# Performance work log

Measured on AMD Instinct MI355X. Metric: run time of the kernel, lower is better.

Reference implementation:

```python
import jax, jax.numpy as jnp
import numpy as np
import math

# dims
H = 2048        # hidden_size
NH = 16         # mamba_num_heads
HPH = 128       # hidden_size_per_head
I = NH * HPH    # intermediate_size = 2048
N = 64          # mamba_d_state
K = 4           # mamba_d_conv
R = max(64, H // 16)  # time_step_rank = 128
L = 2048        # total tokens (single prefill sequence)
EPS = 1e-6


def rmsnorm(x, w, eps=EPS):
    return x * jax.lax.rsqrt(jnp.mean(x * x, axis=-1, keepdims=True) + eps) * w


def setup_inputs() -> dict:
    key = jax.random.key(0)
    ks = jax.random.split(key, 12)
    s = 0.02
    # dt_bias per get_initial_dt_bias
    dt_min, dt_max = 0.001, 0.1
    u = jax.random.uniform(ks[0], (NH,))
    dt = jnp.exp(u * (math.log(dt_max) - math.log(dt_min)) + math.log(dt_min))
    dt = jnp.clip(dt, 0.0001)
    dt_bias = dt + jnp.log(-jnp.expm1(-dt))
    return {
        "hidden_states": jax.random.normal(ks[1], (L, H), jnp.float32),
        "in_proj_w": jax.random.normal(ks[2], (H, 2 * I), jnp.float32) * s,
        "conv_w": jax.random.normal(ks[3], (I, K), jnp.float32) * s,
        "bcdt_w": jax.random.normal(ks[4], (I, 2 * N + R), jnp.float32) * s,
        "dt_norm_w": jnp.ones((R,), jnp.float32),
        "B_norm_w": jnp.ones((N,), jnp.float32),
        "C_norm_w": jnp.ones((N,), jnp.float32),
        "dt_proj_w": jax.random.normal(ks[5], (R, NH), jnp.float32) * s,
        "dt_bias": dt_bias.astype(jnp.float32),
        "A": -jnp.exp(jax.random.normal(ks[6], (I, N), jnp.float32) * 0.5),  # A = -exp(A_log)
        "D": jnp.ones((I,), jnp.float32),
        "out_proj_w": jax.random.normal(ks[7], (I, H), jnp.float32) * s,
    }


def reference(hidden_states, in_proj_w, conv_w, bcdt_w, dt_norm_w, B_norm_w,
              C_norm_w, dt_proj_w, dt_bias, A, D, out_proj_w):
    # in_proj -> [L, NH, 2*HPH]; split into gate and hidden (per-head halves)
    proj = (hidden_states @ in_proj_w).reshape(L, NH, 2 * HPH)
    gate = proj[:, :, :HPH].reshape(L, I)
    hs = proj[:, :, HPH:].reshape(L, I)

    # causal depthwise conv1d along time + SiLU
    xp = jnp.pad(hs, ((K - 1, 0), (0, 0)))  # left-pad time (zero initial conv state)
    conv = sum(conv_w[:, k] * xp[k:k + L] for k in range(K))  # [L, I]
    hs = jax.nn.silu(conv)

    # B, C, dt projections + RMSNorms
    ssm_p = hs @ bcdt_w  # [L, 2N+R]
    B = rmsnorm(ssm_p[:, :N], B_norm_w)          # [L, N]
    C = rmsnorm(ssm_p[:, N:2 * N], C_norm_w)     # [L, N]
    ts = rmsnorm(ssm_p[:, 2 * N:], dt_norm_w)    # [L, R]
    dt = ts @ dt_proj_w                           # [L, NH]

    # expand per-head dt / bias to full intermediate dim, softplus discretization
    dt_full = jnp.repeat(dt, HPH, axis=1)         # [L, I]
    bias_full = jnp.repeat(dt_bias, HPH)          # [I]
    delta = jax.nn.softplus(dt_full + bias_full)  # [L, I]

    # selective scan: state [I, N], zero initial state
    def step(state, xs):
        u_t, d_t, B_t, C_t = xs
        dA = jnp.exp(d_t[:, None] * A)                      # [I, N]
        state = state * dA + (d_t * u_t)[:, None] * B_t[None, :]
        y_t = state @ C_t                                    # [I]
        return state, y_t

    state0 = jnp.zeros((I, N), jnp.float32)
    _, ys = jax.lax.scan(step, state0, (hs, delta, B, C))    # ys: [L, I]

    y = ys + D * hs
    y = y * jax.nn.silu(gate)
    return y @ out_proj_w  # [L, H]
```

## Files before the change

kernel.cpp:

```cpp
#include <hip/hip_runtime.h>
#include <hip/hip_bf16.h>

#define L_   2048
#define H_   2048
#define I_   2048
#define NH_  16
#define HPH_ 128
#define NS_  64
#define R_   128
#define NCH_ 64
#define CT_  32
#define LOG2E 1.4426950408889634f

typedef __attribute__((ext_vector_type(8))) short s16x8;
typedef __attribute__((ext_vector_type(4))) float f32x4;

__device__ __forceinline__ short f2bf(float x) {
  unsigned u = __builtin_bit_cast(unsigned, x);
  u += 0x7fff + ((u >> 16) & 1);
  return (short)(u >> 16);
}
__device__ __forceinline__ float bf2f(unsigned short v) {
  return __builtin_bit_cast(float, (unsigned)v << 16);
}

__device__ __forceinline__ float ex2(float x) {
  return __builtin_amdgcn_exp2f(x);
}

__device__ __forceinline__ void gll16(const void* g, void* l) {
  __builtin_amdgcn_global_load_lds(
      (__attribute__((address_space(1))) void*)(void*)g,
      (__attribute__((address_space(3))) void*)l, 16, 0, 0);
}

__global__ __launch_bounds__(256) void pack_w(const float* __restrict__ W,
                                              short* __restrict__ Wp,
                                              int KN, int logN) {
  int idx = blockIdx.x * 256 + threadIdx.x;
  if (idx >= KN) return;
  int k = idx >> logN;
  int n = idx & ((1 << logN) - 1);
  Wp[((size_t)(k >> 3) << (logN + 3)) + ((size_t)n << 3) + (k & 7)] = f2bf(W[idx]);
}

__global__ __launch_bounds__(256) void cast_bf(const float* __restrict__ X,
                                               short* __restrict__ Xb, int nElem) {
  int idx = blockIdx.x * 256 + threadIdx.x;
  if (idx < nElem) Xb[idx] = f2bf(X[idx]);
}

template<int BM>
__global__ __launch_bounds__(256) void gemm_st(const short* __restrict__ A,
                                               const short* __restrict__ Bp,
                                               float* __restrict__ C,
                                               int M, int N, int K) {
  constexpr int MI = BM / 32;
  __shared__ short sA[BM * 64];
  __shared__ short sB[8 * 128 * 8];
  int tid = threadIdx.x;
  int lane = tid & 63, wid = tid >> 6;
  int wr = wid >> 1, wc = wid & 1;
  int l15 = lane & 15, l16 = lane >> 4;

  int nwg = gridDim.x * gridDim.y;
  int lin = blockIdx.x + gridDim.x * blockIdx.y;
  int cpx = nwg >> 3;
  int swz = (lin & 7) * cpx + (lin >> 3);
  int bm = (swz % gridDim.x) * BM, bn = (swz / gridDim.x) * 128;

  f32x4 acc[MI][4] = {};

  int arow = lane >> 3;
  int acolb = ((lane & 7) ^ arow) * 16;
  const char* Ag = (const char*)(A + (size_t)bm * K) + acolb;
  const char* Bg = (const char*)(Bp + (size_t)bn * 8);

  for (int k0 = 0; k0 < K; k0 += 64) {
    __syncthreads();
#pragma unroll
    for (int q = 0; q < BM / 32; ++q) {
      int rbase = (q * 4 + wid) * 8;
      gll16(Ag + ((size_t)(rbase + arow) * K + k0) * 2,
            (char*)sA + rbase * 128);
    }
#pragma unroll
    for (int q = 0; q < 4; ++q) {
      int c = q * 4 + wid;
      int kg = c >> 1, nh = (c & 1) * 64;
      gll16(Bg + ((size_t)(k0 / 8 + kg) * N * 8 + (size_t)(nh + lane) * 8) * 2,
            (char*)sB + kg * 2048 + nh * 16);
    }
    __syncthreads();

#pragma unroll
    for (int kk = 0; kk < 64; kk += 32) {
      s16x8 a[MI], b[4];
#pragma unroll
      for (int mi = 0; mi < MI; ++mi) {
        int row = wr * (BM / 2) + mi * 16 + l15;
        int kb = ((kk + l16 * 8) * 2) ^ ((row & 7) << 4);
        a[mi] = *(const s16x8*)((const char*)sA + row * 128 + kb);
      }
#pragma unroll
      for (int ni = 0; ni < 4; ++ni) {
        int n = wc * 64 + ni * 16 + l15;
        int kg = (kk >> 3) + l16;
        b[ni] = *(const s16x8*)((const char*)sB + (kg * 128 + n) * 16);
      }
#pragma unroll
      for (int mi = 0; mi < MI; ++mi)
#pragma unroll
        for (int ni = 0; ni < 4; ++ni)
          acc[mi][ni] = __builtin_amdgcn_mfma_f32_16x16x32_bf16(a[mi], b[ni], acc[mi][ni], 0, 0, 0);
    }
  }
#pragma unroll
  for (int mi = 0; mi < MI; ++mi) {
    int row0 = bm + wr * (BM / 2) + mi * 16 + l16 * 4;
#pragma unroll
    for (int ni = 0; ni < 4; ++ni) {
      int col = bn + wc * 64 + ni * 16 + l15;
#pragma unroll
      for (int r = 0; r < 4; ++r)
        C[(size_t)(row0 + r) * N + col] = acc[mi][ni][r];
    }
  }
}

__global__ __launch_bounds__(256) void conv_silu(const float* __restrict__ proj,
                                                 const float* __restrict__ convw,
                                                 float* __restrict__ hs,
                                                 short* __restrict__ hsb,
                                                 float* __restrict__ gate_s) {
  int idx = blockIdx.x * 256 + threadIdx.x;
  int t = idx >> 11, i = idx & (I_ - 1);
  int col = ((i >> 7) << 8) + 128 + (i & 127);
  float4 cw = *(const float4*)(convw + i * 4);
  const float* p = proj + (size_t)t * (2 * I_) + col;
  float acc = cw.w * p[0];
  if (t >= 1) acc += cw.z * p[-(2 * I_)];
  if (t >= 2) acc += cw.y * p[-(2 * I_) * 2];
  if (t >= 3) acc += cw.x * p[-(2 * I_) * 3];
  float h = acc / (1.f + __expf(-acc));
  hs[idx] = h;
  hsb[idx] = f2bf(h);
  float g = p[-128];
  gate_s[idx] = g / (1.f + __expf(-g));
}

__global__ __launch_bounds__(256) void norm_dt(const float* __restrict__ sp,
                                               const float* __restrict__ Bw,
                                               const float* __restrict__ Cw,
                                               const float* __restrict__ dtw,
                                               const float* __restrict__ Wdt,
                                               const float* __restrict__ bias,
                                               float* __restrict__ Bo,
                                               float* __restrict__ Co,
                                               float* __restrict__ delta) {
  int lane = threadIdx.x & 63, w = threadIdx.x >> 6;
  int t = blockIdx.x * 4 + w;
  const float* row = sp + (size_t)t * 256;
  float v0 = row[lane], v1 = row[64 + lane], v2 = row[128 + lane], v3 = row[192 + lane];
  float sB = v0 * v0, sC = v1 * v1, sT = v2 * v2 + v3 * v3;
#pragma unroll
  for (int off = 32; off; off >>= 1) {
    sB += __shfl_xor(sB, off);
    sC += __shfl_xor(sC, off);
    sT += __shfl_xor(sT, off);
  }
  float rB = rsqrtf(sB * (1.f / 64) + 1e-6f);
  float rC = rsqrtf(sC * (1.f / 64) + 1e-6f);
  float rT = rsqrtf(sT * (1.f / 128) + 1e-6f);
  Bo[t * 64 + lane] = v0 * rB * Bw[lane];
  Co[t * 64 + lane] = v1 * rC * Cw[lane];
  float t2 = v2 * rT * dtw[lane], t3 = v3 * rT * dtw[64 + lane];
  float p[NH_];
  const float* w0 = Wdt + lane * NH_;
  const float* w1 = Wdt + (64 + lane) * NH_;
#pragma unroll
  for (int h = 0; h < NH_; ++h) p[h] = t2 * w0[h] + t3 * w1[h];
#pragma unroll
  for (int off = 32; off; off >>= 1)
#pragma unroll
    for (int h = 0; h < NH_; ++h) p[h] += __shfl_xor(p[h], off);
  if (lane == 0) {
#pragma unroll
    for (int h = 0; h < NH_; ++h) {
      float x = p[h] + bias[h];
      delta[t * NH_ + h] = (x > 20.f) ? x : log1pf(__expf(x));
    }
  }
}

__global__ __launch_bounds__(512) void chunk_sums(const float* __restrict__ delta,
                                                  float* __restrict__ sumd) {
  int t = blockIdx.x * 512 + threadIdx.x;
  int c = t >> 4, h = t & 15;
  float s = 0.f;
  const float* p = delta + (size_t)c * CT_ * NH_ + h;
#pragma unroll 8
  for (int j = 0; j < CT_; ++j) s += p[(size_t)j * NH_];
  sumd[t] = s;
}

__device__ __forceinline__ float rdlane(float v, int l) {
  return __builtin_bit_cast(float, __builtin_amdgcn_readlane(__builtin_bit_cast(int, v), l));
}

__global__ __launch_bounds__(256) void scan1(const float* __restrict__ hs,
                                             const float* __restrict__ Bm,
                                             const float* __restrict__ delta,
                                             const float* __restrict__ A,
                                             short* __restrict__ st) {
  __shared__ float sB[CT_ * 64];
  int tid = threadIdx.x;
  int lane = tid & 63, wv = tid >> 6;
  int c0w = blockIdx.x * 256 + wv * 64;
  int c = lane & 15, q = lane >> 4;
  int chunk = blockIdx.y;
  int t0 = chunk * CT_;
  int head = c0w >> 7;
  int nb = q * 16;
  int ch0 = c0w + c;

  { const float4* B4 = (const float4*)(Bm + (size_t)t0 * 64);
    float4* S4 = (float4*)sB;
    S4[tid] = B4[tid];
    S4[256 + tid] = B4[256 + tid]; }
  float d_r = delta[(size_t)(t0 + (lane & 31)) * NH_ + head];

  float aL[4][16], s[4][16];
#pragma unroll
  for (int j = 0; j < 4; ++j) {
    const float* Ap = A + (size_t)(ch0 + 16 * j) * 64 + nb;
#pragma unroll
    for (int k4 = 0; k4 < 4; ++k4) {
      float4 av = *(const float4*)(Ap + k4 * 4);
      aL[j][k4*4+0] = av.x * LOG2E; aL[j][k4*4+1] = av.y * LOG2E;
      aL[j][k4*4+2] = av.z * LOG2E; aL[j][k4*4+3] = av.w * LOG2E;
    }
#pragma unroll
    for (int k = 0; k < 16; ++k) s[j][k] = 0.f;
  }
  __syncthreads();

  const float* up = hs + (size_t)t0 * I_;
  float n0 = up[ch0], n1 = up[ch0 + 16], n2 = up[ch0 + 32], n3 = up[ch0 + 48];
#pragma unroll 1
  for (int t = 0; t < CT_; ++t) {
    float u0 = n0, u1 = n1, u2 = n2, u3 = n3;
    const float* upn = up + (size_t)(t + 1) * I_;
    n0 = upn[ch0]; n1 = upn[ch0 + 16]; n2 = upn[ch0 + 32]; n3 = upn[ch0 + 48];
    float dlt = rdlane(d_r, t);
    float du0 = dlt * u0, du1 = dlt * u1, du2 = dlt * u2, du3 = dlt * u3;
    const float* bt = &sB[t * 64 + nb];
#pragma unroll
    for (int k4 = 0; k4 < 4; ++k4) {
      float4 b4 = *(const float4*)&bt[k4 * 4];
#pragma unroll
      for (int e = 0; e < 4; ++e) {
        int k = k4 * 4 + e; float bb = (&b4.x)[e];
        s[0][k] = s[0][k] * ex2(dlt * aL[0][k]) + du0 * bb;
        s[1][k] = s[1][k] * ex2(dlt * aL[1][k]) + du1 * bb;
        s[2][k] = s[2][k] * ex2(dlt * aL[2][k]) + du2 * bb;
        s[3][k] = s[3][k] * ex2(dlt * aL[3][k]) + du3 * bb;
      }
    }
  }
  size_t base = ((size_t)chunk << 17) + ch0;
#pragma unroll
  for (int j = 0; j < 4; ++j)
#pragma unroll
    for (int k = 0; k < 16; ++k)
      st[base + ((size_t)(nb + k) << 11) + 16 * j] = f2bf(s[j][k]);
}

__global__ __launch_bounds__(256) void scan2(const float* __restrict__ A,
                                             const float* __restrict__ sumd,
                                             short* __restrict__ st) {
  int g = blockIdx.x * 256 + threadIdx.x;
  int i = g & (I_ - 1), n = g >> 11;
  int h = i >> 7;
  float aL = A[((size_t)i << 6) + n] * LOG2E;
  float loc[NCH_];
#pragma unroll
  for (int c = 0; c < NCH_; ++c)
    loc[c] = bf2f((unsigned short)st[((size_t)c << 17) + g]);
  float s = 0.f;
#pragma unroll
  for (int c = 0; c < NCH_; ++c) {
    float gfac = ex2(aL * sumd[c * 16 + h]);
    float nxt = s * gfac + loc[c];
    st[((size_t)c << 17) + g] = f2bf(s);
    s = nxt;
  }
}

__global__ __launch_bounds__(256) void scan3(const float* __restrict__ hs,
                                             const float* __restrict__ Bm,
                                             const float* __restrict__ Cm,
                                             const float* __restrict__ delta,
                                             const float* __restrict__ A,
                                             const float* __restrict__ Dv,
                                             const float* __restrict__ gate_s,
                                             const short* __restrict__ st,
                                             short* __restrict__ ybf) {
  __shared__ float sB[CT_ * 64], sC[CT_ * 64];
  int tid = threadIdx.x;
  int lane = tid & 63, wv = tid >> 6;
  int c0w = blockIdx.x * 256 + wv * 64;
  int c = lane & 15, q = lane >> 4;
  int chunk = blockIdx.y;
  int t0 = chunk * CT_;
  int head = c0w >> 7;
  int nb = q * 16;
  int ch0 = c0w + c;

  { const float4* B4 = (const float4*)(Bm + (size_t)t0 * 64);
    const float4* C4 = (const float4*)(Cm + (size_t)t0 * 64);
    float4* SB4 = (float4*)sB;
    float4* SC4 = (float4*)sC;
    SB4[tid] = B4[tid];       SB4[256 + tid] = B4[256 + tid];
    SC4[tid] = C4[tid];       SC4[256 + tid] = C4[256 + tid]; }
  float d_r = delta[(size_t)(t0 + (lane & 31)) * NH_ + head];
  float D_own = Dv[c0w + lane];

  float aL[4][16], s[4][16];
#pragma unroll
  for (int j = 0; j < 4; ++j) {
    const float* Ap = A + (size_t)(ch0 + 16 * j) * 64 + nb;
#pragma unroll
    for (int k4 = 0; k4 < 4; ++k4) {
      float4 av = *(const float4*)(Ap + k4 * 4);
      aL[j][k4*4+0] = av.x * LOG2E; aL[j][k4*4+1] = av.y * LOG2E;
      aL[j][k4*4+2] = av.z * LOG2E; aL[j][k4*4+3] = av.w * LOG2E;
    }
  }
  { size_t base = ((size_t)chunk << 17) + ch0;
#pragma unroll
    for (int j = 0; j < 4; ++j)
#pragma unroll
      for (int k = 0; k < 16; ++k)
        s[j][k] = bf2f((unsigned short)st[base + ((size_t)(nb + k) << 11) + 16 * j]);
  }
  __syncthreads();

  const float* up = hs + (size_t)t0 * I_;
  const float* gp = gate_s + (size_t)t0 * I_ + c0w + lane;
  short* yp = ybf + (size_t)t0 * I_ + c0w + lane;
  float n0 = up[ch0], n1 = up[ch0 + 16], n2 = up[ch0 + 32], n3 = up[ch0 + 48];
  bool b4f = lane & 16, b5f = lane & 32;
#pragma unroll 1
  for (int t = 0; t < CT_; ++t) {
    float u0 = n0, u1 = n1, u2 = n2, u3 = n3;
    const float* upn = up + (size_t)(t + 1) * I_;
    n0 = upn[ch0]; n1 = upn[ch0 + 16]; n2 = upn[ch0 + 32]; n3 = upn[ch0 + 48];
    float gv = gp[(size_t)t * I_];
    float dlt = rdlane(d_r, t);
    float du0 = dlt * u0, du1 = dlt * u1, du2 = dlt * u2, du3 = dlt * u3;
    const float* bt = &sB[t * 64 + nb];
    const float* ct = &sC[t * 64 + nb];
    float p0 = 0.f, p1 = 0.f, p2 = 0.f, p3 = 0.f;
#pragma unroll
    for (int k4 = 0; k4 < 4; ++k4) {
      float4 b4 = *(const float4*)&bt[k4 * 4];
      float4 c4 = *(const float4*)&ct[k4 * 4];
#pragma unroll
      for (int e = 0; e < 4; ++e) {
        int k = k4 * 4 + e;
        float bb = (&b4.x)[e], cc = (&c4.x)[e];
        s[0][k] = s[0][k] * ex2(dlt * aL[0][k]) + du0 * bb;  p0 += s[0][k] * cc;
        s[1][k] = s[1][k] * ex2(dlt * aL[1][k]) + du1 * bb;  p1 += s[1][k] * cc;
        s[2][k] = s[2][k] * ex2(dlt * aL[2][k]) + du2 * bb;  p2 += s[2][k] * cc;
        s[3][k] = s[3][k] * ex2(dlt * aL[3][k]) + du3 * bb;  p3 += s[3][k] * cc;
      }
    }
    float sa = b5f ? p0 : p2;
    float sb = b5f ? p1 : p3;
    float qa = (b5f ? p2 : p0) + __shfl_xor(sa, 32);
    float qb = (b5f ? p3 : p1) + __shfl_xor(sb, 32);
    float sc = b4f ? qa : qb;
    float y  = (b4f ? qb : qa) + __shfl_xor(sc, 16);
    float u_own = b5f ? (b4f ? u3 : u2) : (b4f ? u1 : u0);
    y += D_own * u_own;
    yp[(size_t)t * I_] = f2bf(y * gv);
  }
}

extern "C" void kernel_launch(void* const* d_in, const int* in_sizes, int n_in,
                              void* d_out, int out_size, void* d_ws, size_t ws_size,
                              hipStream_t stream) {
  const float* hidden  = (const float*)d_in[0];
  const float* inproj  = (const float*)d_in[1];
  const float* convw   = (const float*)d_in[2];
  const float* bcdtw   = (const float*)d_in[3];
  const float* dtnw    = (const float*)d_in[4];
  const float* Bnw     = (const float*)d_in[5];
  const float* Cnw     = (const float*)d_in[6];
  const float* dtpw    = (const float*)d_in[7];
  const float* dtbias  = (const float*)d_in[8];
  const float* Amat    = (const float*)d_in[9];
  const float* Dvec    = (const float*)d_in[10];
  const float* outproj = (const float*)d_in[11];
  float* out = (float*)d_out;

  char* ws = (char*)d_ws;
  short* inproj_p  = (short*)ws; ws += (size_t)H_ * 2 * I_ * 2;
  short* bcdt_p    = (short*)ws; ws += (size_t)I_ * 256 * 2;
  short* outproj_p = (short*)ws; ws += (size_t)I_ * H_ * 2;
  short* hid_b     = (short*)ws; ws += (size_t)L_ * H_ * 2;
  float* proj      = (float*)ws; ws += (size_t)L_ * 2 * I_ * 4;
  float* hs        = (float*)ws; ws += (size_t)(L_ + 1) * I_ * 4;
  short* hs_b      = (short*)ws; ws += (size_t)L_ * I_ * 2;
  float* gate_s    = (float*)ws; ws += (size_t)L_ * I_ * 4;
  float* ssmp      = (float*)ws; ws += (size_t)L_ * 256 * 4;
  float* Bmat      = (float*)ws; ws += (size_t)L_ * NS_ * 4;
  float* Cmat      = (float*)ws; ws += (size_t)L_ * NS_ * 4;
  float* delta     = (float*)ws; ws += (size_t)L_ * NH_ * 4;
  short* y_b       = (short*)ws; ws += (size_t)L_ * I_ * 2;
  float* sumd      = (float*)ws; ws += NCH_ * 16 * 4;
  short* sstate    = (short*)proj;

  pack_w<<<(H_ * 2 * I_ + 255) / 256, 256, 0, stream>>>(inproj, inproj_p, H_ * 2 * I_, 12);
  pack_w<<<(I_ * 256 + 255) / 256, 256, 0, stream>>>(bcdtw, bcdt_p, I_ * 256, 8);
  pack_w<<<(I_ * H_ + 255) / 256, 256, 0, stream>>>(outproj, outproj_p, I_ * H_, 11);
  cast_bf<<<(L_ * H_ + 255) / 256, 256, 0, stream>>>(hidden, hid_b, L_ * H_);

  gemm_st<128><<<dim3(L_ / 128, (2 * I_) / 128), 256, 0, stream>>>(hid_b, inproj_p, proj, L_, 2 * I_, H_);
  conv_silu<<<(L_ * I_) / 256, 256, 0, stream>>>(proj, convw, hs, hs_b, gate_s);
  gemm_st<64><<<dim3(L_ / 64, 256 / 128), 256, 0, stream>>>(hs_b, bcdt_p, ssmp, L_, 256, I_);
  norm_dt<<<L_ / 4, 256, 0, stream>>>(ssmp, Bnw, Cnw, dtnw, dtpw, dtbias, Bmat, Cmat, delta);

  chunk_sums<<<(NCH_ * 16) / 512, 512, 0, stream>>>(delta, sumd);
  scan1<<<dim3(I_ / 256, NCH_), 256, 0, stream>>>(hs, Bmat, delta, Amat, sstate);
  scan2<<<(I_ * 64) / 256, 256, 0, stream>>>(Amat, sumd, sstate);
  scan3<<<dim3(I_ / 256, NCH_), 256, 0, stream>>>(hs, Bmat, Cmat, delta, Amat, Dvec, gate_s, sstate, y_b);

  gemm_st<64><<<dim3(L_ / 64, H_ / 128), 256, 0, stream>>>(y_b, outproj_p, out, L_, H_, I_);
}
```

Before: 277.4 us.

## Halve per-thread state in chunked scan kernels to double thread parallelism

Each wave in scan1 and scan3 now covers 32 channels instead of 64, and each thread holds 8 state elements per channel instead of 16. This halves register use per thread and doubles the number of blocks. scan3's cross-lane reduction is rewritten as a shuffle tree over the 8-lane groups, and only the lower 32 lanes store outputs. The aims are higher occupancy and more latency hiding in the sequential time loop. The costs are redundant loads of B/C/delta per block, more shuffles per output, and half the lanes sitting idle during the store.

```diff
diff --git a/kernel.cpp b/kernel.cpp
--- a/kernel.cpp
+++ b/kernel.cpp
@@ -216,13 +216,13 @@
   __shared__ float sB[CT_ * 64];
   int tid = threadIdx.x;
   int lane = tid & 63, wv = tid >> 6;
-  int c0w = blockIdx.x * 256 + wv * 64;
-  int c = lane & 15, q = lane >> 4;
+  int c0w = blockIdx.x * 128 + wv * 32;
+  int c3 = lane & 7, q = lane >> 3;
   int chunk = blockIdx.y;
   int t0 = chunk * CT_;
   int head = c0w >> 7;
-  int nb = q * 16;
-  int ch0 = c0w + c;
+  int nb = q * 8;
+  int ch0 = c0w + c3;
 
   { const float4* B4 = (const float4*)(Bm + (size_t)t0 * 64);
     float4* S4 = (float4*)sB;
@@ -230,33 +230,33 @@
     S4[256 + tid] = B4[256 + tid]; }
   float d_r = delta[(size_t)(t0 + (lane & 31)) * NH_ + head];
 
-  float aL[4][16], s[4][16];
+  float aL[4][8], s[4][8];
 #pragma unroll
   for (int j = 0; j < 4; ++j) {
-    const float* Ap = A + (size_t)(ch0 + 16 * j) * 64 + nb;
-#pragma unroll
-    for (int k4 = 0; k4 < 4; ++k4) {
+    const float* Ap = A + (size_t)(ch0 + 8 * j) * 64 + nb;
+#pragma unroll
+    for (int k4 = 0; k4 < 2; ++k4) {
       float4 av = *(const float4*)(Ap + k4 * 4);
       aL[j][k4*4+0] = av.x * LOG2E; aL[j][k4*4+1] = av.y * LOG2E;
       aL[j][k4*4+2] = av.z * LOG2E; aL[j][k4*4+3] = av.w * LOG2E;
     }
 #pragma unroll
-    for (int k = 0; k < 16; ++k) s[j][k] = 0.f;
+    for (int k = 0; k < 8; ++k) s[j][k] = 0.f;
   }
   __syncthreads();
 
   const float* up = hs + (size_t)t0 * I_;
-  float n0 = up[ch0], n1 = up[ch0 + 16], n2 = up[ch0 + 32], n3 = up[ch0 + 48];
+  float n0 = up[ch0], n1 = up[ch0 + 8], n2 = up[ch0 + 16], n3 = up[ch0 + 24];
 #pragma unroll 1
   for (int t = 0; t < CT_; ++t) {
     float u0 = n0, u1 = n1, u2 = n2, u3 = n3;
     const float* upn = up + (size_t)(t + 1) * I_;
-    n0 = upn[ch0]; n1 = upn[ch0 + 16]; n2 = upn[ch0 + 32]; n3 = upn[ch0 + 48];
+    n0 = upn[ch0]; n1 = upn[ch0 + 8]; n2 = upn[ch0 + 16]; n3 = upn[ch0 + 24];
     float dlt = rdlane(d_r, t);
     float du0 = dlt * u0, du1 = dlt * u1, du2 = dlt * u2, du3 = dlt * u3;
     const float* bt = &sB[t * 64 + nb];
 #pragma unroll
-    for (int k4 = 0; k4 < 4; ++k4) {
+    for (int k4 = 0; k4 < 2; ++k4) {
       float4 b4 = *(const float4*)&bt[k4 * 4];
 #pragma unroll
       for (int e = 0; e < 4; ++e) {
@@ -272,8 +272,8 @@
 #pragma unroll
   for (int j = 0; j < 4; ++j)
 #pragma unroll
-    for (int k = 0; k < 16; ++k)
-      st[base + ((size_t)(nb + k) << 11) + 16 * j] = f2bf(s[j][k]);
+    for (int k = 0; k < 8; ++k)
+      st[base + ((size_t)(nb + k) << 11) + 8 * j] = f2bf(s[j][k]);
 }
 
 __global__ __launch_bounds__(256) void scan2(const float* __restrict__ A,
@@ -309,13 +309,13 @@
   __shared__ float sB[CT_ * 64], sC[CT_ * 64];
   int tid = threadIdx.x;
   int lane = tid & 63, wv = tid >> 6;
-  int c0w = blockIdx.x * 256 + wv * 64;
-  int c = lane & 15, q = lane >> 4;
+  int c0w = blockIdx.x * 128 + wv * 32;
+  int c3 = lane & 7, q = lane >> 3;
   int chunk = blockIdx.y;
   int t0 = chunk * CT_;
   int head = c0w >> 7;
-  int nb = q * 16;
-  int ch0 = c0w + c;
+  int nb = q * 8;
+  int ch0 = c0w + c3;
 
   { const float4* B4 = (const float4*)(Bm + (size_t)t0 * 64);
     const float4* C4 = (const float4*)(Cm + (size_t)t0 * 64);
@@ -324,14 +324,14 @@
     SB4[tid] = B4[tid];       SB4[256 + tid] = B4[256 + tid];
     SC4[tid] = C4[tid];       SC4[256 + tid] = C4[256 + tid]; }
   float d_r = delta[(size_t)(t0 + (lane & 31)) * NH_ + head];
-  float D_own = Dv[c0w + lane];
-
-  float aL[4][16], s[4][16];
+  float D_own = Dv[c0w + (lane & 31)];
+
+  float aL[4][8], s[4][8];
 #pragma unroll
   for (int j = 0; j < 4; ++j) {
-    const float* Ap = A + (size_t)(ch0 + 16 * j) * 64 + nb;
-#pragma unroll
-    for (int k4 = 0; k4 < 4; ++k4) {
+    const float* Ap = A + (size_t)(ch0 + 8 * j) * 64 + nb;
+#pragma unroll
+    for (int k4 = 0; k4 < 2; ++k4) {
       float4 av = *(const float4*)(Ap + k4 * 4);
       aL[j][k4*4+0] = av.x * LOG2E; aL[j][k4*4+1] = av.y * LOG2E;
       aL[j][k4*4+2] = av.z * LOG2E; aL[j][k4*4+3] = av.w * LOG2E;
@@ -341,21 +341,22 @@
 #pragma unroll
     for (int j = 0; j < 4; ++j)
 #pragma unroll
-      for (int k = 0; k < 16; ++k)
-        s[j][k] = bf2f((unsigned short)st[base + ((size_t)(nb + k) << 11) + 16 * j]);
+      for (int k = 0; k < 8; ++k)
+        s[j][k] = bf2f((unsigned short)st[base + ((size_t)(nb + k) << 11) + 8 * j]);
   }
   __syncthreads();
 
   const float* up = hs + (size_t)t0 * I_;
-  const float* gp = gate_s + (size_t)t0 * I_ + c0w + lane;
-  short* yp = ybf + (size_t)t0 * I_ + c0w + lane;
-  float n0 = up[ch0], n1 = up[ch0 + 16], n2 = up[ch0 + 32], n3 = up[ch0 + 48];
-  bool b4f = lane & 16, b5f = lane & 32;
+  const float* gp = gate_s + (size_t)t0 * I_ + c0w + (lane & 31);
+  short* yp = ybf + (size_t)t0 * I_ + c0w + (lane & 31);
+  float n0 = up[ch0], n1 = up[ch0 + 8], n2 = up[ch0 + 16], n3 = up[ch0 + 24];
+  bool b3f = lane & 8, b4f = lane & 16;
+  int j2 = (lane >> 3) & 3;
 #pragma unroll 1
   for (int t = 0; t < CT_; ++t) {
     float u0 = n0, u1 = n1, u2 = n2, u3 = n3;
     const float* upn = up + (size_t)(t + 1) * I_;
-    n0 = upn[ch0]; n1 = upn[ch0 + 16]; n2 = upn[ch0 + 32]; n3 = upn[ch0 + 48];
+    n0 = upn[ch0]; n1 = upn[ch0 + 8]; n2 = upn[ch0 + 16]; n3 = upn[ch0 + 24];
     float gv = gp[(size_t)t * I_];
     float dlt = rdlane(d_r, t);
     float du0 = dlt * u0, du1 = dlt * u1, du2 = dlt * u2, du3 = dlt * u3;
@@ -363,7 +364,7 @@
     const float* ct = &sC[t * 64 + nb];
     float p0 = 0.f, p1 = 0.f, p2 = 0.f, p3 = 0.f;
 #pragma unroll
-    for (int k4 = 0; k4 < 4; ++k4) {
+    for (int k4 = 0; k4 < 2; ++k4) {
       float4 b4 = *(const float4*)&bt[k4 * 4];
       float4 c4 = *(const float4*)&ct[k4 * 4];
 #pragma unroll
@@ -376,15 +377,19 @@
         s[3][k] = s[3][k] * ex2(dlt * aL[3][k]) + du3 * bb;  p3 += s[3][k] * cc;
       }
     }
-    float sa = b5f ? p0 : p2;
-    float sb = b5f ? p1 : p3;
-    float qa = (b5f ? p2 : p0) + __shfl_xor(sa, 32);
-    float qb = (b5f ? p3 : p1) + __shfl_xor(sb, 32);
-    float sc = b4f ? qa : qb;
-    float y  = (b4f ? qb : qa) + __shfl_xor(sc, 16);
-    float u_own = b5f ? (b4f ? u3 : u2) : (b4f ? u1 : u0);
-    y += D_own * u_own;
-    yp[(size_t)t * I_] = f2bf(y * gv);
+    p0 += __shfl_xor(p0, 8);
+    p1 += __shfl_xor(p1, 8);
+    p2 += __shfl_xor(p2, 8);
+    p3 += __shfl_xor(p3, 8);
+    float q0 = b3f ? p1 : p0;
+    float q1 = b3f ? p3 : p2;
+    q0 += __shfl_xor(q0, 16);
+    q1 += __shfl_xor(q1, 16);
+    float r = b4f ? q1 : q0;
+    r += __shfl_xor(r, 32);
+    float u_own = (j2 == 0) ? u0 : (j2 == 1) ? u1 : (j2 == 2) ? u2 : u3;
+    float y = r + D_own * u_own;
+    if (lane < 32) yp[(size_t)t * I_] = f2bf(y * gv);
   }
 }
 
@@ -433,9 +438,9 @@
   norm_dt<<<L_ / 4, 256, 0, stream>>>(ssmp, Bnw, Cnw, dtnw, dtpw, dtbias, Bmat, Cmat, delta);
 
   chunk_sums<<<(NCH_ * 16) / 512, 512, 0, stream>>>(delta, sumd);
-  scan1<<<dim3(I_ / 256, NCH_), 256, 0, stream>>>(hs, Bmat, delta, Amat, sstate);
+  scan1<<<dim3(I_ / 128, NCH_), 256, 0, stream>>>(hs, Bmat, delta, Amat, sstate);
   scan2<<<(I_ * 64) / 256, 256, 0, stream>>>(Amat, sumd, sstate);
-  scan3<<<dim3(I_ / 256, NCH_), 256, 0, stream>>>(hs, Bmat, Cmat, delta, Amat, Dvec, gate_s, sstate, y_b);
+  scan3<<<dim3(I_ / 128, NCH_), 256, 0, stream>>>(hs, Bmat, Cmat, delta, Amat, Dvec, gate_s, sstate, y_b);
 
   gemm_st<64><<<dim3(L_ / 64, H_ / 128), 256, 0, stream>>>(y_b, outproj_p, out, L_, H_, I_);
 }
```

Measured after the change: 286.2 us (median of 2 runs). 1.03x slower.
